# Kernel optimization log

Hardware: AMD Instinct MI355X
Metric: run time of the kernel (lower is better)

Reference implementation:

```python
import jax, jax.numpy as jnp
import numpy as np

N = 100000      # n_nodes
D = 64          # in_features == out_features (elementwise W mul requires equality)
DEG = 16        # avg degree for random edges
H = 2           # n_head
ALPHA = 0.2     # LeakyReLU negative slope


def setup_inputs() -> dict:
    key = jax.random.key(0)
    k1, k2, k3 = jax.random.split(key, 3)
    inputs = jax.random.normal(k1, (N, D), dtype=jnp.float32)
    # random edges + self-loops so every row has at least one edge (nonzero rowsum)
    rnd = jax.random.randint(k2, (2, N * DEG), 0, N)
    self_loops = jnp.tile(jnp.arange(N)[None, :], (2, 1))
    edge_index = jnp.concatenate([self_loops, rnd], axis=1)  # [2, 1.7M]
    # per-head params, matching torch init: W = ones, a ~ U(-stdv, stdv)
    W = jnp.ones((H, D), dtype=jnp.float32)
    stdv = 1.0 / np.sqrt(D * 2)
    a = jax.random.uniform(k3, (H, 2 * D), dtype=jnp.float32, minval=-stdv, maxval=stdv)
    return {"inputs": inputs, "edge_index": edge_index, "W": W, "a": a}


def reference(inputs, edge_index, W, a):
    n = inputs.shape[0]
    row, col = edge_index[0], edge_index[1]

    def head(Wh, ah):
        h = inputs * Wh  # [N, D]
        # a @ [h_src; h_dst] decomposes into per-node dots, then scalar edge gather
        score = (h @ ah[:D])[row] + (h @ ah[D:])[col]          # [E]
        e = jnp.exp(jnp.where(score > 0, score, ALPHA * score))  # exp(leaky_relu)
        rowsum = jax.ops.segment_sum(e, row, num_segments=n)     # [N]
        # sparse.mm(coo(edge, e), inputs): h_prime[i] = sum_j e_ij * inputs[j]
        h_prime = jax.ops.segment_sum(e[:, None] * inputs[col], row, num_segments=n)
        return h_prime / rowsum[:, None]

    outs = jax.vmap(head)(W, a)  # [H, N, D]
    return outs.mean(axis=0)
```

## Files before the change

kernel.cpp:

```cpp
#include <hip/hip_runtime.h>
#include <hip/hip_fp16.h>


#define D 64
#define ALPHA 0.2f
#define CAP 96
#define BSHIFT 8
#define BROWS 256
#define MAXBUK 512
#define TILE 2048
#define PK2 17
#define M17 ((1u << PK2) - 1u)
#define CAPE 6144
#define SSTR 8192

__device__ __forceinline__ unsigned bf16rne(float f) {
    unsigned u = __float_as_uint(f);
    u += 0x7fffu + ((u >> 16) & 1u);
    return u >> 16;
}
__device__ __forceinline__ float lrexp(float sc) {
    return __expf(sc > 0.f ? sc : ALPHA * sc);
}
__device__ __forceinline__ unsigned packe(float e0, float e1) {
    __half2 h = __floats2half2_rn(e0, e1);
    return *reinterpret_cast<unsigned*>(&h);
}
__device__ __forceinline__ float2 unpacke(unsigned u) {
    __half2 h = *reinterpret_cast<__half2*>(&u);
    return __half22float2(h);
}

__global__ __launch_bounds__(256) void k_front(
    const float* __restrict__ x, const float* __restrict__ W,
    const float* __restrict__ a, float4* __restrict__ s,
    unsigned* __restrict__ xh2, const int* __restrict__ row,
    unsigned short* __restrict__ tcnt, int N, int E, int nblkA)
{
    __shared__ int h[MAXBUK];
    if ((int)blockIdx.x < nblkA) {
        int wid  = (blockIdx.x * 256 + threadIdx.x) >> 6;
        int lane = threadIdx.x & 63;
        int node = wid * 4 + (lane >> 4);
        int f4   = lane & 15;
        if (node >= N) return;
        const float4* x4 = (const float4*)x;
        const float4* W4 = (const float4*)W;
        const float4* A4 = (const float4*)a;
        float4 v  = x4[(size_t)node * 16 + f4];
        unsigned u01 = (bf16rne(v.y) << 16) | bf16rne(v.x);
        unsigned u23 = (bf16rne(v.w) << 16) | bf16rne(v.z);
        *(uint2*)(xh2 + (size_t)node * 32 + 2 * f4) = make_uint2(u01, u23);
        float4 w0 = W4[f4], w1 = W4[16 + f4];
        float4 a0 = A4[f4], a1 = A4[16 + f4], a2 = A4[32 + f4], a3 = A4[48 + f4];
        float t0 = v.x*w0.x*a0.x + v.y*w0.y*a0.y + v.z*w0.z*a0.z + v.w*w0.w*a0.w;
        float t1 = v.x*w0.x*a1.x + v.y*w0.y*a1.y + v.z*w0.z*a1.z + v.w*w0.w*a1.w;
        float t2 = v.x*w1.x*a2.x + v.y*w1.y*a2.y + v.z*w1.z*a2.z + v.w*w1.w*a2.w;
        float t3 = v.x*w1.x*a3.x + v.y*w1.y*a3.y + v.z*w1.z*a3.z + v.w*w1.w*a3.w;
#pragma unroll
        for (int off = 1; off < 16; off <<= 1) {
            t0 += __shfl_xor(t0, off);
            t1 += __shfl_xor(t1, off);
            t2 += __shfl_xor(t2, off);
            t3 += __shfl_xor(t3, off);
        }
        if (f4 == 0) s[node] = make_float4(t0, t1, t2, t3);
    } else {
        int tile = blockIdx.x - nblkA;
        int t = threadIdx.x, base = tile * TILE;
        int cnt = E - base; if (cnt > TILE) cnt = TILE;
        h[t] = 0; h[t + 256] = 0;
        __syncthreads();
        for (int i = t; i < cnt; i += 256) atomicAdd(&h[row[base + i] >> BSHIFT], 1);
        __syncthreads();
        tcnt[(size_t)tile * MAXBUK + t]       = (unsigned short)h[t];
        tcnt[(size_t)tile * MAXBUK + t + 256] = (unsigned short)h[t + 256];
    }
}

__global__ __launch_bounds__(256) void k_binning(
    const int* __restrict__ row, const int* __restrict__ col,
    const unsigned short* __restrict__ tcnt, unsigned* __restrict__ ebuf,
    unsigned* __restrict__ tmeta, int E)
{
    __shared__ unsigned lpk[TILE];
    __shared__ int cur[MAXBUK];
    __shared__ int wsum[256];
    int t = threadIdx.x, tile = blockIdx.x, base = tile * TILE;
    int cnt = E - base; if (cnt > TILE) cnt = TILE;

    int h0 = tcnt[(size_t)tile * MAXBUK + 2 * t];
    int h1 = tcnt[(size_t)tile * MAXBUK + 2 * t + 1];
    int sv = h0 + h1;
    wsum[t] = sv;
    __syncthreads();
    for (int off = 1; off < 256; off <<= 1) {
        int add = (t >= off) ? wsum[t - off] : 0;
        __syncthreads();
        wsum[t] += add;
        __syncthreads();
    }
    int run = wsum[t] - sv;
    cur[2 * t] = run;  cur[2 * t + 1] = run + h0;
    tmeta[(size_t)tile * MAXBUK + 2 * t]     = ((unsigned)run << 16) | (unsigned)h0;
    tmeta[(size_t)tile * MAXBUK + 2 * t + 1] = ((unsigned)(run + h0) << 16) | (unsigned)h1;
    __syncthreads();

    for (int i = t; i < cnt; i += 256) {
        int r = row[base + i], c = col[base + i];
        int p = atomicAdd(&cur[r >> BSHIFT], 1);
        lpk[p] = ((unsigned)(r & (BROWS - 1)) << PK2) | (unsigned)c;
    }
    __syncthreads();
    for (int i = t; i < cnt; i += 256) ebuf[base + i] = lpk[i];
}

__global__ __launch_bounds__(1024) void k_rowsort(
    const unsigned* __restrict__ ebuf, const unsigned* __restrict__ tmeta,
    const float4* __restrict__ s, int* __restrict__ offsets,
    int* __restrict__ counts, unsigned* __restrict__ scol,
    __half* __restrict__ ecoef, int NT, int N)
{
    __shared__ unsigned lpkA[CAPE];
    __shared__ unsigned lpkB[CAPE];
    __shared__ unsigned levB[CAPE];
    __shared__ int   hist[BROWS], offs[BROWS], cursor[BROWS];
    __shared__ float rs0[BROWS], rs1[BROWS], rsx[BROWS], rsz[BROWS];
    __shared__ int   wsum[256];
    __shared__ int   top;
    int b = blockIdx.x, t = threadIdx.x;
    int lo = b << BSHIFT;

    if (t < BROWS) {
        int g = lo + t;
        float4 f = (g < N) ? s[g] : make_float4(0.f, 0.f, 0.f, 0.f);
        rsx[t] = f.x; rsz[t] = f.z;
        hist[t] = 0; rs0[t] = 0.f; rs1[t] = 0.f;
    }
    if (t == 0) top = 0;
    __syncthreads();

    int myh = 0, mybase = 0, mydst = 0;
    if (t < NT) {
        unsigned m = tmeta[(size_t)t * MAXBUK + b];
        myh = (int)(m & 0xffffu);
        mybase = t * TILE + (int)(m >> 16);
        if (myh) mydst = atomicAdd(&top, myh);
    }
    __syncthreads();
    int seg = top;
    size_t ob = (size_t)b * SSTR;

    if (seg <= CAPE) {
        for (int j = 0; j < myh; j++) {
            unsigned pk = ebuf[mybase + j];
            lpkA[mydst + j] = pk;
            atomicAdd(&hist[pk >> PK2], 1);
        }
        __syncthreads();
        int a = 0;
        if (t < 256) { a = hist[t]; wsum[t] = a; }
        __syncthreads();
        for (int off = 1; off < 256; off <<= 1) {
            int add = 0;
            if (t < 256 && t >= off) add = wsum[t - off];
            __syncthreads();
            if (t < 256) wsum[t] += add;
            __syncthreads();
        }
        if (t < 256) { offs[t] = wsum[t] - a; cursor[t] = wsum[t] - a; }
        __syncthreads();
        for (int i = t; i < seg; i += 1024) {
            unsigned pk = lpkA[i];
            int r = pk >> PK2, c = (int)(pk & M17);
            float4 sc = s[c];
            float e0 = lrexp(rsx[r] + sc.y);
            float e1 = lrexp(rsz[r] + sc.w);
            atomicAdd(&rs0[r], e0);
            atomicAdd(&rs1[r], e1);
            int p = atomicAdd(&cursor[r], 1);
            lpkB[p] = pk; levB[p] = packe(e0, e1);
        }
        __syncthreads();
        if (t < BROWS) {
            rs0[t] = 0.5f / rs0[t]; rs1[t] = 0.5f / rs1[t];
            int rg = lo + t;
            if (rg < N) { offsets[rg] = (int)ob + offs[t]; counts[rg] = hist[t]; }
        }
        __syncthreads();
        for (int i = t; i < seg; i += 1024) {
            unsigned pk = lpkB[i];
            int r = pk >> PK2;
            float2 ef = unpacke(levB[i]);
            scol[ob + i]  = (pk & M17) << 5;
            ecoef[ob + i] = __float2half(rs0[r] * ef.x + rs1[r] * ef.y);
        }
    } else {
        for (int j = 0; j < myh; j++) {
            unsigned pk = ebuf[mybase + j];
            int r = pk >> PK2, c = (int)(pk & M17);
            float4 sc = s[c];
            atomicAdd(&rs0[r], lrexp(rsx[r] + sc.y));
            atomicAdd(&rs1[r], lrexp(rsz[r] + sc.w));
            atomicAdd(&hist[r], 1);
        }
        __syncthreads();
        int a = 0;
        if (t < 256) { a = hist[t]; wsum[t] = a; }
        __syncthreads();
        for (int off = 1; off < 256; off <<= 1) {
            int add = 0;
            if (t < 256 && t >= off) add = wsum[t - off];
            __syncthreads();
            if (t < 256) wsum[t] += add;
            __syncthreads();
        }
        if (t < 256) { offs[t] = wsum[t] - a; cursor[t] = wsum[t] - a; }
        __syncthreads();
        if (t < BROWS) {
            rs0[t] = 0.5f / rs0[t]; rs1[t] = 0.5f / rs1[t];
            int rg = lo + t;
            if (rg < N) { offsets[rg] = (int)ob + offs[t]; counts[rg] = hist[t]; }
        }
        __syncthreads();
        for (int j = 0; j < myh; j++) {
            unsigned pk = ebuf[mybase + j];
            int r = pk >> PK2, c = (int)(pk & M17);
            float4 sc = s[c];
            float coef = rs0[r] * lrexp(rsx[r] + sc.y)
                       + rs1[r] * lrexp(rsz[r] + sc.w);
            int p = atomicAdd(&cursor[r], 1);
            if ((unsigned)p < SSTR) {
                scol[ob + p]  = (unsigned)(pk & M17) << 5;
                ecoef[ob + p] = __float2half(coef);
            }
        }
    }
}

__global__ __launch_bounds__(256) void k_gather(
    const unsigned* __restrict__ xh2, const int* __restrict__ offsets,
    const int* __restrict__ counts, const unsigned* __restrict__ scol,
    const __half* __restrict__ ecoef, float* __restrict__ out, int N)
{
    __shared__ unsigned lc[4][CAP];
    __shared__ float    lf[4][CAP];
    int w    = threadIdx.x >> 6;
    int lane = threadIdx.x & 63;
    int n    = blockIdx.x * 4 + w;
    if (n >= N) return;
    int start = offsets[n], cnt = counts[n];
    int m = cnt < CAP ? cnt : CAP;
    for (int k = lane; k < m; k += 64) {
        lc[w][k] = scol[start + k];
        lf[w][k] = __half2float(ecoef[start + k]);
    }
    int mp = (m + 7) & ~7;
    { int k = m + lane; if (k < mp) { lc[w][k] = 0; lf[w][k] = 0.f; } }

    int q  = lane >> 4;
    int li = lane & 15;
    float a0 = 0.f, a1 = 0.f, a2 = 0.f, a3 = 0.f;
    for (int k = 0; k < mp; k += 8) {
#pragma unroll
        for (int j = 0; j < 2; j++) {
            int kk = k + 4 * j + q;
            unsigned cb = lc[w][kk];
            float    cf = lf[w][kk];
            uint2 u = *(const uint2*)(xh2 + cb + 2 * li);
            a0 += cf * __uint_as_float(u.x << 16);
            a1 += cf * __uint_as_float(u.x & 0xffff0000u);
            a2 += cf * __uint_as_float(u.y << 16);
            a3 += cf * __uint_as_float(u.y & 0xffff0000u);
        }
    }
    for (int kk = CAP + q; kk < cnt; kk += 4) {
        unsigned cb = scol[start + kk];
        float    cf = __half2float(ecoef[start + kk]);
        uint2 u = *(const uint2*)(xh2 + cb + 2 * li);
        a0 += cf * __uint_as_float(u.x << 16);
        a1 += cf * __uint_as_float(u.x & 0xffff0000u);
        a2 += cf * __uint_as_float(u.y << 16);
        a3 += cf * __uint_as_float(u.y & 0xffff0000u);
    }
    a0 += __shfl_xor(a0, 16); a0 += __shfl_xor(a0, 32);
    a1 += __shfl_xor(a1, 16); a1 += __shfl_xor(a1, 32);
    a2 += __shfl_xor(a2, 16); a2 += __shfl_xor(a2, 32);
    a3 += __shfl_xor(a3, 16); a3 += __shfl_xor(a3, 32);
    if (q == 0)
        ((float4*)(out + (size_t)n * D))[li] = make_float4(a0, a1, a2, a3);
}

extern "C" void kernel_launch(void* const* d_in, const int* in_sizes, int n_in,
                              void* d_out, int out_size, void* d_ws, size_t ws_size,
                              hipStream_t stream)
{
    const float* x  = (const float*)d_in[0];
    const int*   ei = (const int*)d_in[1];
    const float* W  = (const float*)d_in[2];
    const float* a  = (const float*)d_in[3];
    float*       out = (float*)d_out;
    int N = in_sizes[0] / D;
    int E = in_sizes[1] / 2;
    const int* row = ei;
    const int* col = ei + E;

    int NBUK = (N + BROWS - 1) >> BSHIFT;
    int NT   = (E + TILE - 1) / TILE;

    uintptr_t wp = (uintptr_t)d_ws;
    auto alloc = [&wp](size_t bytes) -> void* {
        wp = (wp + 255) & ~(uintptr_t)255;
        void* p = (void*)wp;
        wp += bytes;
        return p;
    };
    unsigned*       xh2     = (unsigned*)alloc((size_t)N * 32 * 4);
    float4*         s       = (float4*)alloc((size_t)N * sizeof(float4));
    int*            offsets = (int*)alloc((size_t)N * sizeof(int));
    int*            counts  = (int*)alloc((size_t)N * sizeof(int));
    unsigned*       ebuf    = (unsigned*)alloc((size_t)E * sizeof(unsigned));
    unsigned*       scol    = (unsigned*)alloc((size_t)NBUK * SSTR * sizeof(unsigned));
    __half*         ecoef   = (__half*)alloc((size_t)NBUK * SSTR * sizeof(__half));
    unsigned*       tmeta   = (unsigned*)alloc((size_t)NT * MAXBUK * sizeof(unsigned));
    unsigned short* tcnt    = (unsigned short*)alloc((size_t)NT * MAXBUK * 2);

    int nblkA = (N + 15) / 16;
    k_front<<<nblkA + NT, 256, 0, stream>>>(x, W, a, s, xh2, row, tcnt, N, E, nblkA);
    k_binning<<<NT, 256, 0, stream>>>(row, col, tcnt, ebuf, tmeta, E);
    k_rowsort<<<NBUK, 1024, 0, stream>>>(ebuf, tmeta, s, offsets, counts, scol, ecoef, NT, N);
    k_gather<<<(N + 3) / 4, 256, 0, stream>>>(xh2, offsets, counts, scol, ecoef, out, N);
}
```

Baseline: 200.6 us.

## Fuse tile histogram into binning and scatter rowsort output directly to global

The per-tile row-bucket histogram moves out of the front kernel and into the binning kernel. Binning now keeps the row/col values in registers across the count and scatter passes, so row is read once and the tcnt buffer round-trip goes away. The rowsort kernel computes exp scores and row sums while it loads edges, then scatters straight into the global scol/ecoef layout through per-row cursors instead of through a second LDS sorted buffer. This cuts LDS use (CAPE lowered, one array dropped) so occupancy can rise, at the cost of scattered global writes and more segments falling into the slow overflow path.

```diff
diff --git a/kernel.cpp b/kernel.cpp
--- a/kernel.cpp
+++ b/kernel.cpp
@@ -11,7 +11,7 @@
 #define TILE 2048
 #define PK2 17
 #define M17 ((1u << PK2) - 1u)
-#define CAPE 6144
+#define CAPE 5120
 #define SSTR 8192
 
 __device__ __forceinline__ unsigned bf16rne(float f) {
@@ -31,66 +31,65 @@
     return __half22float2(h);
 }
 
-__global__ __launch_bounds__(256) void k_front(
+__global__ __launch_bounds__(256) void k_scores(
     const float* __restrict__ x, const float* __restrict__ W,
     const float* __restrict__ a, float4* __restrict__ s,
-    unsigned* __restrict__ xh2, const int* __restrict__ row,
-    unsigned short* __restrict__ tcnt, int N, int E, int nblkA)
-{
-    __shared__ int h[MAXBUK];
-    if ((int)blockIdx.x < nblkA) {
-        int wid  = (blockIdx.x * 256 + threadIdx.x) >> 6;
-        int lane = threadIdx.x & 63;
-        int node = wid * 4 + (lane >> 4);
-        int f4   = lane & 15;
-        if (node >= N) return;
-        const float4* x4 = (const float4*)x;
-        const float4* W4 = (const float4*)W;
-        const float4* A4 = (const float4*)a;
-        float4 v  = x4[(size_t)node * 16 + f4];
-        unsigned u01 = (bf16rne(v.y) << 16) | bf16rne(v.x);
-        unsigned u23 = (bf16rne(v.w) << 16) | bf16rne(v.z);
-        *(uint2*)(xh2 + (size_t)node * 32 + 2 * f4) = make_uint2(u01, u23);
-        float4 w0 = W4[f4], w1 = W4[16 + f4];
-        float4 a0 = A4[f4], a1 = A4[16 + f4], a2 = A4[32 + f4], a3 = A4[48 + f4];
-        float t0 = v.x*w0.x*a0.x + v.y*w0.y*a0.y + v.z*w0.z*a0.z + v.w*w0.w*a0.w;
-        float t1 = v.x*w0.x*a1.x + v.y*w0.y*a1.y + v.z*w0.z*a1.z + v.w*w0.w*a1.w;
-        float t2 = v.x*w1.x*a2.x + v.y*w1.y*a2.y + v.z*w1.z*a2.z + v.w*w1.w*a2.w;
-        float t3 = v.x*w1.x*a3.x + v.y*w1.y*a3.y + v.z*w1.z*a3.z + v.w*w1.w*a3.w;
+    unsigned* __restrict__ xh2, int N)
+{
+    int wid  = (blockIdx.x * 256 + threadIdx.x) >> 6;
+    int lane = threadIdx.x & 63;
+    int node = wid * 4 + (lane >> 4);
+    int f4   = lane & 15;
+    if (node >= N) return;
+    const float4* x4 = (const float4*)x;
+    const float4* W4 = (const float4*)W;
+    const float4* A4 = (const float4*)a;
+    float4 v  = x4[(size_t)node * 16 + f4];
+    unsigned u01 = (bf16rne(v.y) << 16) | bf16rne(v.x);
+    unsigned u23 = (bf16rne(v.w) << 16) | bf16rne(v.z);
+    *(uint2*)(xh2 + (size_t)node * 32 + 2 * f4) = make_uint2(u01, u23);
+    float4 w0 = W4[f4], w1 = W4[16 + f4];
+    float4 a0 = A4[f4], a1 = A4[16 + f4], a2 = A4[32 + f4], a3 = A4[48 + f4];
+    float t0 = v.x*w0.x*a0.x + v.y*w0.y*a0.y + v.z*w0.z*a0.z + v.w*w0.w*a0.w;
+    float t1 = v.x*w0.x*a1.x + v.y*w0.y*a1.y + v.z*w0.z*a1.z + v.w*w0.w*a1.w;
+    float t2 = v.x*w1.x*a2.x + v.y*w1.y*a2.y + v.z*w1.z*a2.z + v.w*w1.w*a2.w;
+    float t3 = v.x*w1.x*a3.x + v.y*w1.y*a3.y + v.z*w1.z*a3.z + v.w*w1.w*a3.w;
 #pragma unroll
-        for (int off = 1; off < 16; off <<= 1) {
-            t0 += __shfl_xor(t0, off);
-            t1 += __shfl_xor(t1, off);
-            t2 += __shfl_xor(t2, off);
-            t3 += __shfl_xor(t3, off);
-        }
-        if (f4 == 0) s[node] = make_float4(t0, t1, t2, t3);
-    } else {
-        int tile = blockIdx.x - nblkA;
-        int t = threadIdx.x, base = tile * TILE;
-        int cnt = E - base; if (cnt > TILE) cnt = TILE;
-        h[t] = 0; h[t + 256] = 0;
-        __syncthreads();
-        for (int i = t; i < cnt; i += 256) atomicAdd(&h[row[base + i] >> BSHIFT], 1);
-        __syncthreads();
-        tcnt[(size_t)tile * MAXBUK + t]       = (unsigned short)h[t];
-        tcnt[(size_t)tile * MAXBUK + t + 256] = (unsigned short)h[t + 256];
-    }
+    for (int off = 1; off < 16; off <<= 1) {
+        t0 += __shfl_xor(t0, off);
+        t1 += __shfl_xor(t1, off);
+        t2 += __shfl_xor(t2, off);
+        t3 += __shfl_xor(t3, off);
+    }
+    if (f4 == 0) s[node] = make_float4(t0, t1, t2, t3);
 }
 
 __global__ __launch_bounds__(256) void k_binning(
     const int* __restrict__ row, const int* __restrict__ col,
-    const unsigned short* __restrict__ tcnt, unsigned* __restrict__ ebuf,
-    unsigned* __restrict__ tmeta, int E)
+    unsigned* __restrict__ ebuf, unsigned* __restrict__ tmeta, int E)
 {
     __shared__ unsigned lpk[TILE];
+    __shared__ int h[MAXBUK];
     __shared__ int cur[MAXBUK];
     __shared__ int wsum[256];
     int t = threadIdx.x, tile = blockIdx.x, base = tile * TILE;
     int cnt = E - base; if (cnt > TILE) cnt = TILE;
 
-    int h0 = tcnt[(size_t)tile * MAXBUK + 2 * t];
-    int h1 = tcnt[(size_t)tile * MAXBUK + 2 * t + 1];
+    h[t] = 0; h[t + 256] = 0;
+    __syncthreads();
+
+    int r[8], c[8];
+#pragma unroll
+    for (int j = 0; j < 8; j++) {
+        int li = j * 256 + t;
+        if (li < cnt) {
+            r[j] = row[base + li]; c[j] = col[base + li];
+            atomicAdd(&h[r[j] >> BSHIFT], 1);
+        } else r[j] = -1;
+    }
+    __syncthreads();
+
+    int h0 = h[2 * t], h1 = h[2 * t + 1];
     int sv = h0 + h1;
     wsum[t] = sv;
     __syncthreads();
@@ -106,10 +105,12 @@
     tmeta[(size_t)tile * MAXBUK + 2 * t + 1] = ((unsigned)(run + h0) << 16) | (unsigned)h1;
     __syncthreads();
 
-    for (int i = t; i < cnt; i += 256) {
-        int r = row[base + i], c = col[base + i];
-        int p = atomicAdd(&cur[r >> BSHIFT], 1);
-        lpk[p] = ((unsigned)(r & (BROWS - 1)) << PK2) | (unsigned)c;
+#pragma unroll
+    for (int j = 0; j < 8; j++) {
+        if (r[j] >= 0) {
+            int p = atomicAdd(&cur[r[j] >> BSHIFT], 1);
+            lpk[p] = ((unsigned)(r[j] & (BROWS - 1)) << PK2) | (unsigned)c[j];
+        }
     }
     __syncthreads();
     for (int i = t; i < cnt; i += 256) ebuf[base + i] = lpk[i];
@@ -122,8 +123,7 @@
     __half* __restrict__ ecoef, int NT, int N)
 {
     __shared__ unsigned lpkA[CAPE];
-    __shared__ unsigned lpkB[CAPE];
-    __shared__ unsigned levB[CAPE];
+    __shared__ unsigned levA[CAPE];
     __shared__ int   hist[BROWS], offs[BROWS], cursor[BROWS];
     __shared__ float rs0[BROWS], rs1[BROWS], rsx[BROWS], rsz[BROWS];
     __shared__ int   wsum[256];
@@ -154,8 +154,15 @@
     if (seg <= CAPE) {
         for (int j = 0; j < myh; j++) {
             unsigned pk = ebuf[mybase + j];
+            int r = pk >> PK2, c = (int)(pk & M17);
+            float4 sc = s[c];
+            float e0 = lrexp(rsx[r] + sc.y);
+            float e1 = lrexp(rsz[r] + sc.w);
+            atomicAdd(&rs0[r], e0);
+            atomicAdd(&rs1[r], e1);
+            atomicAdd(&hist[r], 1);
             lpkA[mydst + j] = pk;
-            atomicAdd(&hist[pk >> PK2], 1);
+            levA[mydst + j] = packe(e0, e1);
         }
         __syncthreads();
         int a = 0;
@@ -170,18 +177,6 @@
         }
         if (t < 256) { offs[t] = wsum[t] - a; cursor[t] = wsum[t] - a; }
         __syncthreads();
-        for (int i = t; i < seg; i += 1024) {
-            unsigned pk = lpkA[i];
-            int r = pk >> PK2, c = (int)(pk & M17);
-            float4 sc = s[c];
-            float e0 = lrexp(rsx[r] + sc.y);
-            float e1 = lrexp(rsz[r] + sc.w);
-            atomicAdd(&rs0[r], e0);
-            atomicAdd(&rs1[r], e1);
-            int p = atomicAdd(&cursor[r], 1);
-            lpkB[p] = pk; levB[p] = packe(e0, e1);
-        }
-        __syncthreads();
         if (t < BROWS) {
             rs0[t] = 0.5f / rs0[t]; rs1[t] = 0.5f / rs1[t];
             int rg = lo + t;
@@ -189,11 +184,13 @@
         }
         __syncthreads();
         for (int i = t; i < seg; i += 1024) {
-            unsigned pk = lpkB[i];
+            unsigned pk = lpkA[i];
             int r = pk >> PK2;
-            float2 ef = unpacke(levB[i]);
-            scol[ob + i]  = (pk & M17) << 5;
-            ecoef[ob + i] = __float2half(rs0[r] * ef.x + rs1[r] * ef.y);
+            float2 ef = unpacke(levA[i]);
+            float coef = rs0[r] * ef.x + rs1[r] * ef.y;
+            int p = atomicAdd(&cursor[r], 1);
+            scol[ob + p]  = (pk & M17) << 5;
+            ecoef[ob + p] = __float2half(coef);
         }
     } else {
         for (int j = 0; j < myh; j++) {
@@ -315,19 +312,17 @@
         wp += bytes;
         return p;
     };
-    unsigned*       xh2     = (unsigned*)alloc((size_t)N * 32 * 4);
-    float4*         s       = (float4*)alloc((size_t)N * sizeof(float4));
-    int*            offsets = (int*)alloc((size_t)N * sizeof(int));
-    int*            counts  = (int*)alloc((size_t)N * sizeof(int));
-    unsigned*       ebuf    = (unsigned*)alloc((size_t)E * sizeof(unsigned));
-    unsigned*       scol    = (unsigned*)alloc((size_t)NBUK * SSTR * sizeof(unsigned));
-    __half*         ecoef   = (__half*)alloc((size_t)NBUK * SSTR * sizeof(__half));
-    unsigned*       tmeta   = (unsigned*)alloc((size_t)NT * MAXBUK * sizeof(unsigned));
-    unsigned short* tcnt    = (unsigned short*)alloc((size_t)NT * MAXBUK * 2);
-
-    int nblkA = (N + 15) / 16;
-    k_front<<<nblkA + NT, 256, 0, stream>>>(x, W, a, s, xh2, row, tcnt, N, E, nblkA);
-    k_binning<<<NT, 256, 0, stream>>>(row, col, tcnt, ebuf, tmeta, E);
+    unsigned* xh2     = (unsigned*)alloc((size_t)N * 32 * 4);
+    float4*   s       = (float4*)alloc((size_t)N * sizeof(float4));
+    int*      offsets = (int*)alloc((size_t)N * sizeof(int));
+    int*      counts  = (int*)alloc((size_t)N * sizeof(int));
+    unsigned* ebuf    = (unsigned*)alloc((size_t)E * sizeof(unsigned));
+    unsigned* scol    = (unsigned*)alloc((size_t)NBUK * SSTR * sizeof(unsigned));
+    __half*   ecoef   = (__half*)alloc((size_t)NBUK * SSTR * sizeof(__half));
+    unsigned* tmeta   = (unsigned*)alloc((size_t)NT * MAXBUK * sizeof(unsigned));
+
+    k_scores<<<(N + 15) / 16, 256, 0, stream>>>(x, W, a, s, xh2, N);
+    k_binning<<<NT, 256, 0, stream>>>(row, col, ebuf, tmeta, E);
     k_rowsort<<<NBUK, 1024, 0, stream>>>(ebuf, tmeta, s, offsets, counts, scol, ecoef, NT, N);
     k_gather<<<(N + 3) / 4, 256, 0, stream>>>(xh2, offsets, counts, scol, ecoef, out, N);
 }
```

Result: slower. 219.8 us (+9.6%).
